# Optimization experiments

Hardware: AMD Instinct MI355X
Metric: run time of the kernel (lower is better)

Reference implementation:

```python
import jax, jax.numpy as jnp
import numpy as np

IN_F, OUT_F, H = 128, 256, 4
D = OUT_F // H  # head_dim = 64
NEG_SLOPE = 0.2


def setup_inputs() -> dict:
    key = jax.random.key(0)
    k1, k2, k3, k4 = jax.random.split(key, 4)
    B, N = 8, 1024
    node_features = jax.random.normal(k1, (B, N, IN_F), dtype=jnp.float32)
    adjacency_matrix = jax.random.randint(k2, (B, N, N), 0, 2, dtype=jnp.int32)
    # W: torch Linear(in,out,bias=False) weight is [out,in]; store as [in,out] for x @ W
    W = jax.random.normal(k3, (IN_F, OUT_F), dtype=jnp.float32) * (1.0 / np.sqrt(IN_F))
    # attention: Linear(2*head_dim, 1, bias=False) -> vector of length 2*D, shared across heads
    a = jax.random.normal(k4, (2 * D,), dtype=jnp.float32) * (1.0 / np.sqrt(2 * D))
    return {"node_features": node_features, "adjacency_matrix": adjacency_matrix, "W": W, "a": a}


def reference(node_features, adjacency_matrix, W, a):
    B, N, _ = node_features.shape
    h = (node_features @ W).reshape(B, N, H, D)  # [B,N,H,D]
    # attention(concat(h_i, h_j)) == <h_i, a[:D]> + <h_j, a[D:]> (same math, no [B,N,N,H,2D] concat)
    s_i = jnp.einsum('bnhd,d->bnh', h, a[:D])  # score contrib of target node i
    s_j = jnp.einsum('bnhd,d->bnh', h, a[D:])  # score contrib of source node j
    e = s_i[:, :, None, :] + s_j[:, None, :, :]  # [B,N,N,H]
    e = jnp.where(e >= 0, e, NEG_SLOPE * e)  # LeakyReLU(0.2)
    mask = adjacency_matrix[..., None] != 0  # [B,N,N,1] -> broadcast over heads
    e = jnp.where(mask, e, -jnp.inf)
    alpha = jax.nn.softmax(e, axis=2)  # softmax over source nodes j
    out = jnp.einsum('bijh,bjhd->bihd', alpha, h)  # weighted sum over j
    return out.reshape(B, N, OUT_F)  # concat=True
```

## Files before the change

### kernel.cpp

```cpp
#include <hip/hip_runtime.h>
#include <math.h>

constexpr int IN_F = 128, OUT_F = 256, NH = 4, HD = 64;
constexpr int B = 8, N = 1024;
#define NEG 0.2f

typedef __attribute__((ext_vector_type(8))) short bf16x8;
typedef __attribute__((ext_vector_type(4))) float f32x4;
typedef __attribute__((ext_vector_type(8))) unsigned short u16x8;

static __device__ __forceinline__ short f2bf(float f) {
    union { float f; unsigned u; } v; v.f = f;
    unsigned r = (v.u + 0x7FFF + ((v.u >> 16) & 1)) >> 16;
    return (short)r;
}

__global__ __launch_bounds__(256) void k_gemm(
    const float* __restrict__ x,
    const float* __restrict__ W,
    const float* __restrict__ a,
    unsigned short* __restrict__ hT,
    float* __restrict__ siT,
    float* __restrict__ sjT)
{
    constexpr int ROWS = 8;
    __shared__ float xs[ROWS][IN_F];
    const int t = threadIdx.x;
    const int row0 = blockIdx.x * ROWS;

    ((float4*)xs)[t] = ((const float4*)(x + (size_t)row0 * IN_F))[t];
    __syncthreads();

    float acc[ROWS];
#pragma unroll
    for (int r = 0; r < ROWS; ++r) acc[r] = 0.f;
    for (int k = 0; k < IN_F; ++k) {
        const float w = W[k * OUT_F + t];
#pragma unroll
        for (int r = 0; r < ROWS; ++r) acc[r] = fmaf(xs[r][k], w, acc[r]);
    }

    const int lane = t & 63, head = t >> 6, d = t & 63;
    const int b = row0 >> 10, n0 = row0 & (N - 1);

    u16x8 pk;
#pragma unroll
    for (int r = 0; r < ROWS; ++r) pk[r] = (unsigned short)f2bf(acc[r]);
    *(u16x8*)&hT[((size_t)(b * NH + head) * HD + d) * N + n0] = pk;

    const float ai = a[lane], aj = a[HD + lane];
#pragma unroll
    for (int r = 0; r < ROWS; ++r) {
        float si = acc[r] * ai;
        float sj = acc[r] * aj;
#pragma unroll
        for (int off = 32; off; off >>= 1) {
            si += __shfl_xor(si, off, 64);
            sj += __shfl_xor(sj, off, 64);
        }
        if (lane == 0) {
            siT[(size_t)(b * NH + head) * N + n0 + r] = si;
            sjT[(size_t)(b * NH + head) * N + n0 + r] = sj;
        }
    }
}

__global__ __launch_bounds__(256) void k_pv(
    const unsigned short* __restrict__ hT,
    const float* __restrict__ siT,
    const float* __restrict__ sjT,
    const int* __restrict__ adj,
    float* __restrict__ out)
{
    constexpr int TJ = 64, NIT = N / TJ, PADJ = 72;
    __shared__ __align__(16) short ht[2][64 * PADJ];
    __shared__ float sjs[N];
    __shared__ float zbuf[4][16];

    const int bid = blockIdx.x;
    const int itile = bid & 15, h = (bid >> 4) & 3, b = bid >> 6;
    const int t = threadIdx.x, lane = t & 63, w = t >> 6;
    const int i0 = itile * 64 + w * 16;

    ((float4*)sjs)[t] = ((const float4*)(sjT + (size_t)(b * NH + h) * N))[t];

    const int il = lane & 15, q = lane >> 4;
    const int i = i0 + il;
    const float si = siT[(size_t)(b * NH + h) * N + i];
    const int4* __restrict__ arow = (const int4*)(adj + ((size_t)b * N + i) * N);
    const unsigned short* __restrict__ hTb = hT + (size_t)(b * NH + h) * HD * N;

    const int srow = t >> 2, sc = (t & 3) * 16;
    const unsigned short* __restrict__ hsrc = hTb + (size_t)srow * N + sc;

    f32x4 acc0 = {0.f,0.f,0.f,0.f}, acc1 = {0.f,0.f,0.f,0.f};
    f32x4 acc2 = {0.f,0.f,0.f,0.f}, acc3 = {0.f,0.f,0.f,0.f};
    float psum = 0.f;
    const int qc = q * 8;

    u16x8 ha = *(const u16x8*)(hsrc);
    u16x8 hc = *(const u16x8*)(hsrc + 8);
    int4 ma0 = arow[qc >> 2];
    int4 ma1 = arow[(qc >> 2) + 1];
    int4 mb0 = arow[(32 + qc) >> 2];
    int4 mb1 = arow[((32 + qc) >> 2) + 1];

    __syncthreads();

    for (int itr = 0; itr < NIT; ++itr) {
        const int j0 = itr * TJ;

        short* __restrict__ hd = &ht[itr & 1][srow * PADJ + sc];
        *(u16x8*)hd = ha;
        *(u16x8*)(hd + 8) = hc;

        const int jn = (j0 + TJ) & (N - 1);
        const u16x8 na = *(const u16x8*)(hsrc + jn);
        const u16x8 nc = *(const u16x8*)(hsrc + jn + 8);
        const int4 xa0 = arow[(jn + qc) >> 2];
        const int4 xa1 = arow[((jn + qc) >> 2) + 1];
        const int4 xb0 = arow[(jn + 32 + qc) >> 2];
        const int4 xb1 = arow[((jn + 32 + qc) >> 2) + 1];

        __syncthreads();

        const short* __restrict__ hbuf = ht[itr & 1];

        {
            const int jq = j0 + qc;
            const float4 s0 = *(const float4*)&sjs[jq];
            const float4 s1 = *(const float4*)&sjs[jq + 4];
            const float sv[8] = {s0.x,s0.y,s0.z,s0.w,s1.x,s1.y,s1.z,s1.w};
            const int   mv[8] = {ma0.x,ma0.y,ma0.z,ma0.w,ma1.x,ma1.y,ma1.z,ma1.w};
            bf16x8 af;
#pragma unroll
            for (int e = 0; e < 8; ++e) {
                float ev = si + sv[e];
                ev = (ev >= 0.f) ? ev : NEG * ev;
                const float pe = (mv[e] != 0) ? __expf(ev) : 0.f;
                psum += pe;
                af[e] = f2bf(pe);
            }
            const bf16x8 b0 = *(const bf16x8*)&hbuf[(0 * 16 + il) * PADJ + qc];
            const bf16x8 b1 = *(const bf16x8*)&hbuf[(1 * 16 + il) * PADJ + qc];
            const bf16x8 b2 = *(const bf16x8*)&hbuf[(2 * 16 + il) * PADJ + qc];
            const bf16x8 b3 = *(const bf16x8*)&hbuf[(3 * 16 + il) * PADJ + qc];
            acc0 = __builtin_amdgcn_mfma_f32_16x16x32_bf16(af, b0, acc0, 0, 0, 0);
            acc1 = __builtin_amdgcn_mfma_f32_16x16x32_bf16(af, b1, acc1, 0, 0, 0);
            acc2 = __builtin_amdgcn_mfma_f32_16x16x32_bf16(af, b2, acc2, 0, 0, 0);
            acc3 = __builtin_amdgcn_mfma_f32_16x16x32_bf16(af, b3, acc3, 0, 0, 0);
        }
        {
            const int jq = j0 + 32 + qc;
            const float4 s0 = *(const float4*)&sjs[jq];
            const float4 s1 = *(const float4*)&sjs[jq + 4];
            const float sv[8] = {s0.x,s0.y,s0.z,s0.w,s1.x,s1.y,s1.z,s1.w};
            const int   mv[8] = {mb0.x,mb0.y,mb0.z,mb0.w,mb1.x,mb1.y,mb1.z,mb1.w};
            bf16x8 af;
#pragma unroll
            for (int e = 0; e < 8; ++e) {
                float ev = si + sv[e];
                ev = (ev >= 0.f) ? ev : NEG * ev;
                const float pe = (mv[e] != 0) ? __expf(ev) : 0.f;
                psum += pe;
                af[e] = f2bf(pe);
            }
            const bf16x8 b0 = *(const bf16x8*)&hbuf[(0 * 16 + il) * PADJ + 32 + qc];
            const bf16x8 b1 = *(const bf16x8*)&hbuf[(1 * 16 + il) * PADJ + 32 + qc];
            const bf16x8 b2 = *(const bf16x8*)&hbuf[(2 * 16 + il) * PADJ + 32 + qc];
            const bf16x8 b3 = *(const bf16x8*)&hbuf[(3 * 16 + il) * PADJ + 32 + qc];
            acc0 = __builtin_amdgcn_mfma_f32_16x16x32_bf16(af, b0, acc0, 0, 0, 0);
            acc1 = __builtin_amdgcn_mfma_f32_16x16x32_bf16(af, b1, acc1, 0, 0, 0);
            acc2 = __builtin_amdgcn_mfma_f32_16x16x32_bf16(af, b2, acc2, 0, 0, 0);
            acc3 = __builtin_amdgcn_mfma_f32_16x16x32_bf16(af, b3, acc3, 0, 0, 0);
        }

        ha = na; hc = nc; ma0 = xa0; ma1 = xa1; mb0 = xb0; mb1 = xb1;
    }

    psum += __shfl_xor(psum, 16, 64);
    psum += __shfl_xor(psum, 32, 64);
    if (lane < 16) zbuf[w][lane] = psum;
    __syncthreads();

    float iz[4];
#pragma unroll
    for (int r = 0; r < 4; ++r) iz[r] = 1.f / zbuf[w][q * 4 + r];

    float* __restrict__ ob = out + ((size_t)b * N + i0) * OUT_F + h * HD + il;
#pragma unroll
    for (int r = 0; r < 4; ++r) {
        float* o = ob + (size_t)(q * 4 + r) * OUT_F;
        o[0]  = acc0[r] * iz[r];
        o[16] = acc1[r] * iz[r];
        o[32] = acc2[r] * iz[r];
        o[48] = acc3[r] * iz[r];
    }
}

extern "C" void kernel_launch(void* const* d_in, const int* in_sizes, int n_in,
                              void* d_out, int out_size, void* d_ws, size_t ws_size,
                              hipStream_t stream) {
    const float* x   = (const float*)d_in[0];
    const int*   adj = (const int*)d_in[1];
    const float* W   = (const float*)d_in[2];
    const float* a   = (const float*)d_in[3];
    float* out = (float*)d_out;

    unsigned short* hT = (unsigned short*)d_ws;
    float* siT = (float*)(hT + (size_t)B * NH * HD * N);
    float* sjT = siT + (size_t)B * NH * N;

    k_gemm<<<B * N / 8, 256, 0, stream>>>(x, W, a, hT, siT, sjT);
    k_pv<<<B * NH * (N / 64), 256, 0, stream>>>(hT, siT, sjT, adj, out);
}
```

Measured before the change: 47.41 us.

## Load h fragments directly from global into registers, drop LDS staging and barriers

The P·V kernel no longer stages the bf16 h tile through double-buffered shared memory with a per-iteration __syncthreads. Each wave now loads its MFMA B-operand fragments straight from global memory into registers, prefetched one iteration ahead. This removes the LDS traffic and block barriers, but the four waves in a block now each fetch the same h data, which raises global/L2 traffic and register pressure. It also adds a launch-bounds occupancy hint of 2 and swaps the hand-rolled float-to-bf16 rounding for the library intrinsic.

```diff
diff --git a/kernel.cpp b/kernel.cpp
--- a/kernel.cpp
+++ b/kernel.cpp
@@ -1,4 +1,5 @@
 #include <hip/hip_runtime.h>
+#include <hip/hip_bf16.h>
 #include <math.h>
 
 constexpr int IN_F = 128, OUT_F = 256, NH = 4, HD = 64;
@@ -10,9 +11,8 @@
 typedef __attribute__((ext_vector_type(8))) unsigned short u16x8;
 
 static __device__ __forceinline__ short f2bf(float f) {
-    union { float f; unsigned u; } v; v.f = f;
-    unsigned r = (v.u + 0x7FFF + ((v.u >> 16) & 1)) >> 16;
-    return (short)r;
+    __hip_bfloat16 b = __float2bfloat16(f);
+    return *reinterpret_cast<short*>(&b);
 }
 
 __global__ __launch_bounds__(256) void k_gemm(
@@ -65,15 +65,14 @@
     }
 }
 
-__global__ __launch_bounds__(256) void k_pv(
+__global__ __launch_bounds__(256, 2) void k_pv(
     const unsigned short* __restrict__ hT,
     const float* __restrict__ siT,
     const float* __restrict__ sjT,
     const int* __restrict__ adj,
     float* __restrict__ out)
 {
-    constexpr int TJ = 64, NIT = N / TJ, PADJ = 72;
-    __shared__ __align__(16) short ht[2][64 * PADJ];
+    constexpr int TJ = 64, NIT = N / TJ;
     __shared__ float sjs[N];
     __shared__ float zbuf[4][16];
 
@@ -84,54 +83,55 @@
 
     ((float4*)sjs)[t] = ((const float4*)(sjT + (size_t)(b * NH + h) * N))[t];
 
-    const int il = lane & 15, q = lane >> 4;
+    const int il = lane & 15, q = lane >> 4, qc = q * 8;
     const int i = i0 + il;
     const float si = siT[(size_t)(b * NH + h) * N + i];
     const int4* __restrict__ arow = (const int4*)(adj + ((size_t)b * N + i) * N);
-    const unsigned short* __restrict__ hTb = hT + (size_t)(b * NH + h) * HD * N;
-
-    const int srow = t >> 2, sc = (t & 3) * 16;
-    const unsigned short* __restrict__ hsrc = hTb + (size_t)srow * N + sc;
+    const unsigned short* __restrict__ hrow =
+        hT + (size_t)(b * NH + h) * HD * N + (size_t)il * N + qc;
 
     f32x4 acc0 = {0.f,0.f,0.f,0.f}, acc1 = {0.f,0.f,0.f,0.f};
     f32x4 acc2 = {0.f,0.f,0.f,0.f}, acc3 = {0.f,0.f,0.f,0.f};
     float psum = 0.f;
-    const int qc = q * 8;
-
-    u16x8 ha = *(const u16x8*)(hsrc);
-    u16x8 hc = *(const u16x8*)(hsrc + 8);
-    int4 ma0 = arow[qc >> 2];
-    int4 ma1 = arow[(qc >> 2) + 1];
-    int4 mb0 = arow[(32 + qc) >> 2];
-    int4 mb1 = arow[((32 + qc) >> 2) + 1];
+
+    bf16x8 cb00 = *(const bf16x8*)(hrow + 0 * 16 * N);
+    bf16x8 cb01 = *(const bf16x8*)(hrow + 1 * 16 * N);
+    bf16x8 cb02 = *(const bf16x8*)(hrow + 2 * 16 * N);
+    bf16x8 cb03 = *(const bf16x8*)(hrow + 3 * 16 * N);
+    bf16x8 cb10 = *(const bf16x8*)(hrow + 0 * 16 * N + 32);
+    bf16x8 cb11 = *(const bf16x8*)(hrow + 1 * 16 * N + 32);
+    bf16x8 cb12 = *(const bf16x8*)(hrow + 2 * 16 * N + 32);
+    bf16x8 cb13 = *(const bf16x8*)(hrow + 3 * 16 * N + 32);
+    int4 cm00 = arow[qc >> 2];
+    int4 cm01 = arow[(qc >> 2) + 1];
+    int4 cm10 = arow[(32 + qc) >> 2];
+    int4 cm11 = arow[((32 + qc) >> 2) + 1];
 
     __syncthreads();
 
     for (int itr = 0; itr < NIT; ++itr) {
         const int j0 = itr * TJ;
-
-        short* __restrict__ hd = &ht[itr & 1][srow * PADJ + sc];
-        *(u16x8*)hd = ha;
-        *(u16x8*)(hd + 8) = hc;
-
         const int jn = (j0 + TJ) & (N - 1);
-        const u16x8 na = *(const u16x8*)(hsrc + jn);
-        const u16x8 nc = *(const u16x8*)(hsrc + jn + 8);
-        const int4 xa0 = arow[(jn + qc) >> 2];
-        const int4 xa1 = arow[((jn + qc) >> 2) + 1];
-        const int4 xb0 = arow[(jn + 32 + qc) >> 2];
-        const int4 xb1 = arow[((jn + 32 + qc) >> 2) + 1];
-
-        __syncthreads();
-
-        const short* __restrict__ hbuf = ht[itr & 1];
+
+        const bf16x8 nb00 = *(const bf16x8*)(hrow + 0 * 16 * N + jn);
+        const bf16x8 nb01 = *(const bf16x8*)(hrow + 1 * 16 * N + jn);
+        const bf16x8 nb02 = *(const bf16x8*)(hrow + 2 * 16 * N + jn);
+        const bf16x8 nb03 = *(const bf16x8*)(hrow + 3 * 16 * N + jn);
+        const bf16x8 nb10 = *(const bf16x8*)(hrow + 0 * 16 * N + jn + 32);
+        const bf16x8 nb11 = *(const bf16x8*)(hrow + 1 * 16 * N + jn + 32);
+        const bf16x8 nb12 = *(const bf16x8*)(hrow + 2 * 16 * N + jn + 32);
+        const bf16x8 nb13 = *(const bf16x8*)(hrow + 3 * 16 * N + jn + 32);
+        const int4 nm00 = arow[(jn + qc) >> 2];
+        const int4 nm01 = arow[((jn + qc) >> 2) + 1];
+        const int4 nm10 = arow[(jn + 32 + qc) >> 2];
+        const int4 nm11 = arow[((jn + 32 + qc) >> 2) + 1];
 
         {
             const int jq = j0 + qc;
             const float4 s0 = *(const float4*)&sjs[jq];
             const float4 s1 = *(const float4*)&sjs[jq + 4];
             const float sv[8] = {s0.x,s0.y,s0.z,s0.w,s1.x,s1.y,s1.z,s1.w};
-            const int   mv[8] = {ma0.x,ma0.y,ma0.z,ma0.w,ma1.x,ma1.y,ma1.z,ma1.w};
+            const int   mv[8] = {cm00.x,cm00.y,cm00.z,cm00.w,cm01.x,cm01.y,cm01.z,cm01.w};
             bf16x8 af;
 #pragma unroll
             for (int e = 0; e < 8; ++e) {
@@ -141,21 +141,17 @@
                 psum += pe;
                 af[e] = f2bf(pe);
             }
-            const bf16x8 b0 = *(const bf16x8*)&hbuf[(0 * 16 + il) * PADJ + qc];
-            const bf16x8 b1 = *(const bf16x8*)&hbuf[(1 * 16 + il) * PADJ + qc];
-            const bf16x8 b2 = *(const bf16x8*)&hbuf[(2 * 16 + il) * PADJ + qc];
-            const bf16x8 b3 = *(const bf16x8*)&hbuf[(3 * 16 + il) * PADJ + qc];
-            acc0 = __builtin_amdgcn_mfma_f32_16x16x32_bf16(af, b0, acc0, 0, 0, 0);
-            acc1 = __builtin_amdgcn_mfma_f32_16x16x32_bf16(af, b1, acc1, 0, 0, 0);
-            acc2 = __builtin_amdgcn_mfma_f32_16x16x32_bf16(af, b2, acc2, 0, 0, 0);
-            acc3 = __builtin_amdgcn_mfma_f32_16x16x32_bf16(af, b3, acc3, 0, 0, 0);
+            acc0 = __builtin_amdgcn_mfma_f32_16x16x32_bf16(af, cb00, acc0, 0, 0, 0);
+            acc1 = __builtin_amdgcn_mfma_f32_16x16x32_bf16(af, cb01, acc1, 0, 0, 0);
+            acc2 = __builtin_amdgcn_mfma_f32_16x16x32_bf16(af, cb02, acc2, 0, 0, 0);
+            acc3 = __builtin_amdgcn_mfma_f32_16x16x32_bf16(af, cb03, acc3, 0, 0, 0);
         }
         {
             const int jq = j0 + 32 + qc;
             const float4 s0 = *(const float4*)&sjs[jq];
             const float4 s1 = *(const float4*)&sjs[jq + 4];
             const float sv[8] = {s0.x,s0.y,s0.z,s0.w,s1.x,s1.y,s1.z,s1.w};
-            const int   mv[8] = {mb0.x,mb0.y,mb0.z,mb0.w,mb1.x,mb1.y,mb1.z,mb1.w};
+            const int   mv[8] = {cm10.x,cm10.y,cm10.z,cm10.w,cm11.x,cm11.y,cm11.z,cm11.w};
             bf16x8 af;
 #pragma unroll
             for (int e = 0; e < 8; ++e) {
@@ -165,17 +161,15 @@
                 psum += pe;
                 af[e] = f2bf(pe);
             }
-            const bf16x8 b0 = *(const bf16x8*)&hbuf[(0 * 16 + il) * PADJ + 32 + qc];
-            const bf16x8 b1 = *(const bf16x8*)&hbuf[(1 * 16 + il) * PADJ + 32 + qc];
-            const bf16x8 b2 = *(const bf16x8*)&hbuf[(2 * 16 + il) * PADJ + 32 + qc];
-            const bf16x8 b3 = *(const bf16x8*)&hbuf[(3 * 16 + il) * PADJ + 32 + qc];
-            acc0 = __builtin_amdgcn_mfma_f32_16x16x32_bf16(af, b0, acc0, 0, 0, 0);
-            acc1 = __builtin_amdgcn_mfma_f32_16x16x32_bf16(af, b1, acc1, 0, 0, 0);
-            acc2 = __builtin_amdgcn_mfma_f32_16x16x32_bf16(af, b2, acc2, 0, 0, 0);
-            acc3 = __builtin_amdgcn_mfma_f32_16x16x32_bf16(af, b3, acc3, 0, 0, 0);
-        }
-
-        ha = na; hc = nc; ma0 = xa0; ma1 = xa1; mb0 = xb0; mb1 = xb1;
+            acc0 = __builtin_amdgcn_mfma_f32_16x16x32_bf16(af, cb10, acc0, 0, 0, 0);
+            acc1 = __builtin_amdgcn_mfma_f32_16x16x32_bf16(af, cb11, acc1, 0, 0, 0);
+            acc2 = __builtin_amdgcn_mfma_f32_16x16x32_bf16(af, cb12, acc2, 0, 0, 0);
+            acc3 = __builtin_amdgcn_mfma_f32_16x16x32_bf16(af, cb13, acc3, 0, 0, 0);
+        }
+
+        cb00 = nb00; cb01 = nb01; cb02 = nb02; cb03 = nb03;
+        cb10 = nb10; cb11 = nb11; cb12 = nb12; cb13 = nb13;
+        cm00 = nm00; cm01 = nm01; cm10 = nm10; cm11 = nm11;
     }
 
     psum += __shfl_xor(psum, 16, 64);
```

Result: slower. 70.90 us (+49.5%).
